# Performance work log

Hardware: AMD Instinct MI355X
Metric: run time of the kernel (lower is better)

Reference implementation:

```python
import jax, jax.numpy as jnp
import numpy as np

B, T, D, L, M = 32, 512, 512, 1024, 10


def setup_inputs() -> dict:
    key = jax.random.key(0)
    ks = jax.random.split(key, 9)
    s = 1.0 / np.sqrt(D)  # torch default uniform init bound
    u = lambda k, sh: jax.random.uniform(k, sh, jnp.float32, -s, s)
    return {
        "input_h_c": jax.random.normal(ks[0], (B, T, D), jnp.float32),
        "memory": jax.random.normal(ks[1], (B, L, D), jnp.float32),
        "input_lengths": jax.random.randint(ks[2], (B,), 1, L + 1),
        "W_ih": u(ks[3], (4 * D, 2 * D)),
        "W_hh": u(ks[4], (4 * D, D)),
        "b_ih": u(ks[5], (4 * D,)),
        "b_hh": u(ks[6], (4 * D,)),
        "W_g": u(ks[7], (3 * M, D)),
        "b_g": u(ks[8], (3 * M,)),
    }


def reference(input_h_c, memory, input_lengths, W_ih, W_hh, b_ih, b_hh, W_g, b_g):
    Bq, Tq, Dq = input_h_c.shape
    Lq = memory.shape[1]
    Mq = b_g.shape[0] // 3
    u_pos = jnp.arange(Lq, dtype=memory.dtype)  # [L]

    def step(carry, x_t):
        h, c, ctx, _ = carry
        x = jnp.concatenate([x_t, ctx], axis=-1)  # [B, 2D]
        gates = x @ W_ih.T + b_ih + h @ W_hh.T + b_hh  # [B, 4D]
        i, f, g, o = jnp.split(gates, 4, axis=-1)  # torch LSTMCell gate order i,f,g,o
        c_n = jax.nn.sigmoid(f) * c + jax.nn.sigmoid(i) * jnp.tanh(g)
        h_n = jax.nn.sigmoid(o) * jnp.tanh(c_n)
        # GMM CDF location attention
        phi = h_n @ W_g.T + b_g  # [B, 3M]
        ksi = jnp.exp(phi[:, :Mq])
        beta = jnp.exp(phi[:, Mq:2 * Mq])
        alpha = jax.nn.softmax(phi[:, 2 * Mq:], axis=-1)
        # 1/(1+exp((ksi-u)/beta)) == sigmoid((u-ksi)/beta)
        cdf = lambda ub: jnp.sum(
            alpha[..., None] * jax.nn.sigmoid((ub - ksi[..., None]) / beta[..., None]),
            axis=1)  # [B, L]
        t1 = cdf(u_pos + 0.5)
        w = t1 - cdf(u_pos - 0.5)  # [B, L]
        ctx_n = jnp.einsum('bl,bld->bd', w, memory)
        return (h_n, c_n, ctx_n, 1.0 - t1), w

    z = jnp.zeros((Bq, Dq), input_h_c.dtype)
    term0 = jnp.zeros((Bq, Lq), input_h_c.dtype)
    (h, c, ctx, term), ws = jax.lax.scan(step, (z, z, z, term0),
                                         jnp.swapaxes(input_h_c, 0, 1))
    alignment = jnp.swapaxes(ws, 0, 1)  # [B, T, L]
    termination = jnp.take_along_axis(term, (input_lengths - 1)[:, None], axis=1)  # [B,1]
    return ctx[:, None, :], alignment, termination
```

## Files before the change

kernel.cpp:

```cpp
#include <hip/hip_runtime.h>

#define Bz 32
#define Tz 512
#define Dz 512
#define Lz 1024
#define Mz 10
#define G4D 2048
#define FP 32
#define NBQ 4
#define NBLK (Bz*NBQ)
#define OFF_FQ   0
#define OFF_HX   4096
#define OFF_WQ   36864
#define OFF_M2   561152
#define OFF_XW   34115584
#define NEED_I   50892800
#define PM 128
#define PN 128
#define PK 32

typedef unsigned long long u64;
typedef unsigned u32;
typedef _Float16 f16x8 __attribute__((ext_vector_type(8)));
typedef float f32x4 __attribute__((ext_vector_type(4)));
typedef _Float16 half2_t __attribute__((ext_vector_type(2)));

#if defined(__has_builtin)
#if __has_builtin(__builtin_amdgcn_fdot2)
#define HAS_FDOT2 1
#endif
#endif

__device__ __forceinline__ float fsig(float x) { return 1.0f / (1.0f + __expf(-x)); }
__device__ __forceinline__ int ld_rlx(const int* p) {
  return __hip_atomic_load(p, __ATOMIC_RELAXED, __HIP_MEMORY_SCOPE_AGENT);
}
__device__ __forceinline__ void st_rlx(int* p, int v) {
  __hip_atomic_store(p, v, __ATOMIC_RELAXED, __HIP_MEMORY_SCOPE_AGENT);
}
__device__ __forceinline__ float ld_rlxf(const float* p) {
  return __hip_atomic_load(p, __ATOMIC_RELAXED, __HIP_MEMORY_SCOPE_AGENT);
}
__device__ __forceinline__ void st_rlxf(float* p, float v) {
  __hip_atomic_store(p, v, __ATOMIC_RELAXED, __HIP_MEMORY_SCOPE_AGENT);
}
__device__ __forceinline__ u32 pack16(float a, float b) {
  unsigned short la = __builtin_bit_cast(unsigned short, (_Float16)a);
  unsigned short lb = __builtin_bit_cast(unsigned short, (_Float16)b);
  return (u32)la | ((u32)lb << 16);
}
__device__ __forceinline__ float lo16(u32 v) {
  return (float)__builtin_bit_cast(half2_t, v)[0];
}
__device__ __forceinline__ float hi16(u32 v) {
  return (float)__builtin_bit_cast(half2_t, v)[1];
}
__device__ __forceinline__ float dot2f(u32 xu, u32 wu, float acc) {
  half2_t xh = __builtin_bit_cast(half2_t, xu);
  half2_t wh = __builtin_bit_cast(half2_t, wu);
#ifdef HAS_FDOT2
  return __builtin_amdgcn_fdot2(xh, wh, acc, false);
#else
  return acc + (float)xh[0]*(float)wh[0] + (float)xh[1]*(float)wh[1];
#endif
}
#define VWAIT() asm volatile("s_waitcnt vmcnt(0)" ::: "memory")

__global__ __launch_bounds__(256) void k_pre(
    const float* __restrict__ x, const float* __restrict__ W_ih,
    const float* __restrict__ b_ih, const float* __restrict__ b_hh,
    u32* __restrict__ xwu)
{
  __shared__ float As[PM][PK+1];
  __shared__ float Bs[PN][PK+1];
  const int m0 = blockIdx.x*PM, n0 = blockIdx.y*PN;
  const int tid = threadIdx.x;
  const int mg = tid >> 4, ng = tid & 15;
  float acc[8][8] = {};
  for (int k0 = 0; k0 < Dz; k0 += PK) {
    for (int i = tid; i < PM*(PK/4); i += 256) {
      int row = i >> 3, c4 = (i & 7) << 2;
      float4 v = *reinterpret_cast<const float4*>(&x[(size_t)(m0+row)*Dz + k0 + c4]);
      As[row][c4] = v.x; As[row][c4+1] = v.y; As[row][c4+2] = v.z; As[row][c4+3] = v.w;
    }
    for (int i = tid; i < PN*(PK/4); i += 256) {
      int row = i >> 3, c4 = (i & 7) << 2;
      float4 v = *reinterpret_cast<const float4*>(&W_ih[(size_t)(n0+row)*(2*Dz) + k0 + c4]);
      Bs[row][c4] = v.x; Bs[row][c4+1] = v.y; Bs[row][c4+2] = v.z; Bs[row][c4+3] = v.w;
    }
    __syncthreads();
    #pragma unroll 8
    for (int k = 0; k < PK; k++) {
      float a8[8], b8[8];
      #pragma unroll
      for (int r = 0; r < 8; r++) a8[r] = As[mg*8+r][k];
      #pragma unroll
      for (int s = 0; s < 8; s++) b8[s] = Bs[ng*8+s][k];
      #pragma unroll
      for (int r = 0; r < 8; r++)
        #pragma unroll
        for (int s = 0; s < 8; s++) acc[r][s] += a8[r]*b8[s];
    }
    __syncthreads();
  }
  const int nb = n0 + ng*8;
  #pragma unroll
  for (int r = 0; r < 8; r++) {
    int m = m0 + mg*8 + r;
    #pragma unroll
    for (int s2 = 0; s2 < 4; s2++) {
      int n = nb + 2*s2;
      xwu[(size_t)m*1024 + (n >> 1)] =
          pack16(acc[r][2*s2]   + b_ih[n]   + b_hh[n],
                 acc[r][2*s2+1] + b_ih[n+1] + b_hh[n+1]);
    }
  }
}

__global__ __launch_bounds__(512) void k_m2(
    const float* __restrict__ memory, const float* __restrict__ W_ih,
    u32* __restrict__ M2u)
{
  __shared__ __align__(16) u32 smem[149760/4];
  u32* Bs = smem;
  u32* As = smem + 33280;
  const int tid = threadIdx.x;
  const int n0 = blockIdx.x * 128, mc = blockIdx.y;
  for (int i = tid; i < 128*256; i += 512) {
    int jl = i >> 8, ku = i & 255;
    float2 wv = *reinterpret_cast<const float2*>(&W_ih[(size_t)(n0+jl)*(2*Dz) + 512 + 2*ku]);
    Bs[jl*260 + (ku ^ ((jl & 7) << 2))] = pack16(wv.x, wv.y);
  }
  __syncthreads();
  const int w = tid >> 6, lane = tid & 63;
  const int fr = lane & 15, kq = (lane >> 4) << 2;
  const int frsw = (fr & 7) << 2;
  for (int mt = 0; mt < 128; ++mt) {
    const int m0 = mc*2048 + mt*16;
    for (int i = tid; i < 16*256; i += 512) {
      int r = i >> 8, ku = i & 255;
      float2 mv = *reinterpret_cast<const float2*>(&memory[(size_t)(m0+r)*Dz + 2*ku]);
      As[r*260 + (ku ^ ((r & 7) << 2))] = pack16(mv.x, mv.y);
    }
    __syncthreads();
    f32x4 acc = {0.f, 0.f, 0.f, 0.f};
    #pragma unroll
    for (int ks = 0; ks < 16; ++ks) {
      int col = (kq + ks*16) ^ frsw;
      f16x8 av = *reinterpret_cast<const f16x8*>(As + fr*260 + col);
      f16x8 bv = *reinterpret_cast<const f16x8*>(Bs + (w*16 + fr)*260 + col);
      acc = __builtin_amdgcn_mfma_f32_16x16x32_f16(av, bv, acc, 0, 0, 0);
    }
    #pragma unroll
    for (int i = 0; i < 4; ++i) {
      float oth = __shfl_xor(acc[i], 1);
      if (!(lane & 1)) {
        int m = m0 + ((lane >> 4) << 2) + i;
        int j = n0 + w*16 + fr;
        M2u[(size_t)m*1024 + (j >> 1)] = pack16(acc[i], oth);
      }
    }
    __syncthreads();
  }
}

__global__ __launch_bounds__(512) void k_packh(
    const float* __restrict__ W_hh, u32* __restrict__ Wq)
{
  const int kp = blockIdx.x;
  for (int idx = threadIdx.x; idx < 2048; idx += 512) {
    int q = idx >> 9, pos = idx & 511;
    int g = pos >> 7, jj = pos & 127;
    int j = 512*g + 128*q + jj;
    float2 wv = *reinterpret_cast<const float2*>(&W_hh[(size_t)j*Dz + 2*kp]);
    Wq[(((size_t)q*256 + kp) << 9) + pos] = pack16(wv.x, wv.y);
  }
}

__global__ __launch_bounds__(512) void k_persist(
    const float* __restrict__ memory, const int* __restrict__ lens,
    const float* __restrict__ W_g,  const float* __restrict__ b_g,
    const u32* __restrict__ xwu, const u32* __restrict__ M2u,
    const u32* __restrict__ Wq,
    float* __restrict__ hx, int* __restrict__ fQ,
    float* __restrict__ ctx_out, float* __restrict__ align_out,
    float* __restrict__ term_out)
{
  const int blk = blockIdx.x, tid = threadIdx.x;
  const int b = blk >> 2, q = blk & 3;

  __shared__ float pgemv[4][512];
  __shared__ float gctxl[512];
  __shared__ float wsm[Lz];
  __shared__ float hf[Dz];
  __shared__ float cs[128];
  __shared__ u32   xp[256];
  __shared__ float2 pg2[2][256];
  __shared__ float phis[3*Mz], prm[3*Mz], lom[Mz], him[Mz];
  __shared__ int rng[2];

  if (tid < 128) cs[tid] = 0.f;
  if (tid < 256) xp[tid] = 0u;
  for (int i = tid; i < 512; i += 512) gctxl[i] = 0.f;
  __syncthreads();

  const uint4* wq4 = reinterpret_cast<const uint4*>(Wq) + (size_t)q*32768;
  const int kg = tid >> 7, tq = tid & 127;

  for (int t = 0; t < Tz; ++t) {
    {
      const uint4* wr = wq4 + tq;
      float a0 = 0.f, a1 = 0.f, a2 = 0.f, a3 = 0.f;
      const int k0 = kg << 6;
      #pragma unroll 4
      for (int kp = k0; kp < k0 + 64; ++kp) {
        uint4 wv = wr[(size_t)kp << 7];
        u32 xv = xp[kp];
        a0 = dot2f(xv, wv.x, a0);
        a1 = dot2f(xv, wv.y, a1);
        a2 = dot2f(xv, wv.z, a2);
        a3 = dot2f(xv, wv.w, a3);
      }
      *reinterpret_cast<float4*>(&pgemv[kg][tq << 2]) = make_float4(a0, a1, a2, a3);
    }
    __syncthreads();

    if (tid < 128) {
      const int dl = tid;
      const size_t xwb = ((size_t)(b*Tz + t)) << 10;
      float gv[4];
      #pragma unroll
      for (int g = 0; g < 4; ++g) {
        int pos = (g << 7) + dl;
        float s = pgemv[0][pos] + pgemv[1][pos] + pgemv[2][pos] + pgemv[3][pos]
                + gctxl[pos];
        int j = (g << 9) + (q << 7) + dl;
        u32 xv = xwu[xwb + (j >> 1)];
        s += (j & 1) ? hi16(xv) : lo16(xv);
        gv[g] = s;
      }
      float ig = fsig(gv[0]);
      float fg = fsig(gv[1]);
      float gg = tanhf(gv[2]);
      float og = fsig(gv[3]);
      float cn = fg*cs[dl] + ig*gg;
      float hn = og*tanhf(cn);
      cs[dl] = cn;
      hf[(q << 7) + dl] = hn;
      st_rlxf(&hx[(((t & 1)*Bz + b)*NBQ + q)*128 + dl], hn);
    }
    VWAIT();
    __syncthreads();
    if (tid == 0) st_rlx(&fQ[(b*NBQ + q)*FP], t+1);

    if (tid < NBQ) {
      while (ld_rlx(&fQ[(b*NBQ + tid)*FP]) < t+1) __builtin_amdgcn_s_sleep(1);
    }
    __syncthreads();
    if (tid < 384) {
      int rp = tid >> 7;
      int p = rp + (rp >= q ? 1 : 0);
      int dl2 = tid & 127;
      hf[(p << 7) + dl2] = ld_rlxf(&hx[(((t & 1)*Bz + b)*NBQ + p)*128 + dl2]);
    }
    __syncthreads();
    if (tid < 256) xp[tid] = pack16(hf[2*tid], hf[2*tid+1]);

    if (tid < 16*3*Mz) {
      int m = tid >> 4, l16 = tid & 15;
      const float4* wr = reinterpret_cast<const float4*>(W_g + m*Dz);
      const float4* hr = reinterpret_cast<const float4*>(hf);
      float s = 0.f;
      #pragma unroll
      for (int i = 0; i < 8; i++) {
        float4 wv = wr[l16 + (i<<4)];
        float4 hv = hr[l16 + (i<<4)];
        s += wv.x*hv.x + wv.y*hv.y + wv.z*hv.z + wv.w*hv.w;
      }
      s += __shfl_xor(s, 1);
      s += __shfl_xor(s, 2);
      s += __shfl_xor(s, 4);
      s += __shfl_xor(s, 8);
      if (l16 == 0) phis[m] = s + b_g[m];
    }
    __syncthreads();

    if (tid < Mz) {
      float ks = expf(phis[tid]);
      float be = expf(phis[Mz + tid]);
      prm[tid]      = ks;
      prm[Mz + tid] = expf(-phis[Mz + tid]);
      lom[tid] = ks - 0.5f - 25.f*be;
      him[tid] = ks + 0.5f + 25.f*be;
    }
    __syncthreads();
    if (tid == 0) {
      float mx = -1e30f;
      #pragma unroll
      for (int m = 0; m < Mz; m++) mx = fmaxf(mx, phis[2*Mz + m]);
      float ae[Mz], ssum = 0.f;
      #pragma unroll
      for (int m = 0; m < Mz; m++) { ae[m] = expf(phis[2*Mz + m] - mx); ssum += ae[m]; }
      float lo = 1e30f, hi = -1e30f;
      #pragma unroll
      for (int m = 0; m < Mz; m++) {
        prm[2*Mz + m] = ae[m] / ssum;
        lo = fminf(lo, lom[m]); hi = fmaxf(hi, him[m]);
      }
      int llo = lo > 0.f ? (int)floorf(lo) : 0;
      if (llo > Lz) llo = Lz;
      int lhi = hi < (float)Lz ? (int)ceilf(hi) + 1 : Lz;
      if (lhi > Lz) lhi = Lz;
      rng[0] = llo; rng[1] = lhi;
    }
    __syncthreads();
    const int llo = rng[0], lhi = rng[1];

    for (int l = llo + tid; l < lhi; l += 512) {
      float u = (float)l;
      float t1 = 0.f, t0 = 0.f;
      #pragma unroll
      for (int m = 0; m < Mz; m++) {
        float ks = prm[m], ib = prm[Mz + m], al = prm[2*Mz + m];
        t1 += al * fsig((u + 0.5f - ks) * ib);
        t0 += al * fsig((u - 0.5f - ks) * ib);
      }
      wsm[l] = t1 - t0;
    }
    __syncthreads();

    if (t < Tz-1) {
      {
        const int seg = tid >> 8, tc = tid & 255;
        const int g = tc >> 6, jj2 = tc & 63;
        const int col = (g << 8) + (q << 6) + jj2;
        const u32* m2c = M2u + (((size_t)b << 10) << 10) + col;
        float alo = 0.f, ahi = 0.f;
        for (int l = llo + seg; l < lhi; l += 2) {
          float wl = wsm[l];
          u32 v = m2c[(size_t)l << 10];
          alo = fmaf(wl, lo16(v), alo);
          ahi = fmaf(wl, hi16(v), ahi);
        }
        pg2[seg][tc] = make_float2(alo, ahi);
      }
      __syncthreads();
      if (tid < 256) {
        float2 v0 = pg2[0][tid], v1 = pg2[1][tid];
        int g = tid >> 6, jj2 = tid & 63;
        gctxl[(g << 7) + 2*jj2]     = v0.x + v1.x;
        gctxl[(g << 7) + 2*jj2 + 1] = v0.y + v1.y;
      }
      __syncthreads();
    } else if (q == 0) {
      {
        const int grp = tid >> 7, d0 = (tid & 127) << 2;
        const float* mb = memory + (size_t)b*Lz*Dz + d0;
        float4 a = make_float4(0.f, 0.f, 0.f, 0.f);
        for (int l = llo + grp; l < lhi; l += 4) {
          float wl = wsm[l];
          float4 m0 = *reinterpret_cast<const float4*>(&mb[(size_t)l*Dz]);
          a.x = fmaf(wl, m0.x, a.x); a.y = fmaf(wl, m0.y, a.y);
          a.z = fmaf(wl, m0.z, a.z); a.w = fmaf(wl, m0.w, a.w);
        }
        *reinterpret_cast<float4*>(&pgemv[grp][d0]) = a;
      }
      __syncthreads();
      ctx_out[b*Dz + tid] = pgemv[0][tid] + pgemv[1][tid] + pgemv[2][tid] + pgemv[3][tid];
      if (tid == 0) {
        float u = (float)(lens[b] - 1);
        float t1 = 0.f;
        #pragma unroll
        for (int m = 0; m < Mz; m++)
          t1 += prm[2*Mz + m] * fsig((u + 0.5f - prm[m]) * prm[Mz + m]);
        term_out[b] = 1.0f - t1;
      }
    }

    if (q == 0) {
      for (int l = llo + tid; l < lhi; l += 512)
        align_out[((size_t)b*Tz + t)*Lz + l] = wsm[l];
    }
  }
}

__global__ __launch_bounds__(256) void k_gemm(
    const float* __restrict__ x_all, const float* __restrict__ ctxs,
    const float* __restrict__ h, const float* __restrict__ W_ih,
    const float* __restrict__ W_hh, float* __restrict__ partial, int t)
{
  __shared__ float Xs[Bz][130];
  __shared__ float Wt[128][130];
  const int jt = blockIdx.x, kcb = blockIdx.y;
  const int j0 = jt*128, k0 = kcb*128;
  const int tid = threadIdx.x;
  for (int i = tid; i < Bz*128; i += 256) {
    int bb = i >> 7, kk = i & 127;
    int k = k0 + kk;
    float v;
    if (k < Dz)        v = x_all[((size_t)bb*Tz + t)*Dz + k];
    else if (k < 2*Dz) v = ctxs[bb*Dz + (k - Dz)];
    else               v = h[bb*Dz + (k - 2*Dz)];
    Xs[bb][kk] = v;
  }
  {
    const float* Wsrc; int ldw, col0;
    if (k0 < 2*Dz) { Wsrc = W_ih; ldw = 2*Dz; col0 = k0; }
    else           { Wsrc = W_hh; ldw = Dz;   col0 = k0 - 2*Dz; }
    for (int i = tid; i < 128*32; i += 256) {
      int jj = i >> 5, k4 = (i & 31) << 2;
      float4 v = *reinterpret_cast<const float4*>(&Wsrc[(size_t)(j0 + jj)*ldw + col0 + k4]);
      Wt[jj][k4] = v.x; Wt[jj][k4+1] = v.y; Wt[jj][k4+2] = v.z; Wt[jj][k4+3] = v.w;
    }
  }
  __syncthreads();
  const int jg = tid & 31, bg = tid >> 5;
  const int bl = bg << 2;
  float acc[4][4] = {};
  #pragma unroll 4
  for (int k = 0; k < 128; k += 2) {
    float2 xv[4], wv[4];
    #pragma unroll
    for (int b2 = 0; b2 < 4; b2++)
      xv[b2] = *reinterpret_cast<const float2*>(&Xs[bl + b2][k]);
    #pragma unroll
    for (int jj = 0; jj < 4; jj++)
      wv[jj] = *reinterpret_cast<const float2*>(&Wt[jg + (jj << 5)][k]);
    #pragma unroll
    for (int jj = 0; jj < 4; jj++)
      #pragma unroll
      for (int b2 = 0; b2 < 4; b2++)
        acc[jj][b2] += wv[jj].x * xv[b2].x + wv[jj].y * xv[b2].y;
  }
  #pragma unroll
  for (int jj = 0; jj < 4; jj++)
    #pragma unroll
    for (int b2 = 0; b2 < 4; b2++)
      partial[((size_t)kcb*Bz + (bl + b2))*G4D + j0 + jg + (jj << 5)] = acc[jj][b2];
}

__global__ __launch_bounds__(512) void k_fused(
    const float* __restrict__ partial, const float* __restrict__ b_ih,
    const float* __restrict__ b_hh,
    float* __restrict__ h, float* __restrict__ c,
    const float* __restrict__ W_g, const float* __restrict__ b_g,
    const float* __restrict__ memory, const int* __restrict__ lens,
    float* __restrict__ ctxs, float* __restrict__ ctx_out,
    float* __restrict__ align_out, float* __restrict__ term_out,
    int t, int final_, int nkc)
{
  const int b = blockIdx.x, tid = threadIdx.x;
  __shared__ float4 gs4[G4D/4];
  __shared__ float hsb[Dz];
  __shared__ float phis[3*Mz];
  __shared__ float prm[3*Mz];
  __shared__ float wsm[Lz];
  __shared__ int   rng[2];
  float* gs = (float*)gs4;
  {
    int j = 4*tid;
    float4 bi = *reinterpret_cast<const float4*>(&b_ih[j]);
    float4 bh = *reinterpret_cast<const float4*>(&b_hh[j]);
    float4 s = make_float4(bi.x+bh.x, bi.y+bh.y, bi.z+bh.z, bi.w+bh.w);
    const float4* pp = reinterpret_cast<const float4*>(partial) + (size_t)b*(G4D/4) + tid;
    for (int kcb = 0; kcb < nkc; kcb++) {
      float4 p = pp[(size_t)kcb*Bz*(G4D/4)];
      s.x += p.x; s.y += p.y; s.z += p.z; s.w += p.w;
    }
    gs4[tid] = s;
  }
  __syncthreads();
  {
    const int d = tid;
    float ig = 1.0f / (1.0f + expf(-gs[d]));
    float fg = 1.0f / (1.0f + expf(-gs[Dz + d]));
    float gg = tanhf(gs[2*Dz + d]);
    float og = 1.0f / (1.0f + expf(-gs[3*Dz + d]));
    float cn = fg * c[b*Dz + d] + ig * gg;
    float hn = og * tanhf(cn);
    c[b*Dz + d] = cn;
    h[b*Dz + d] = hn;
    hsb[d] = hn;
  }
  __syncthreads();
  if (tid < 16*3*Mz) {
    int m = tid >> 4, l16 = tid & 15;
    float s = 0.f;
    #pragma unroll 4
    for (int k = l16; k < Dz; k += 16) s += W_g[m*Dz + k] * hsb[k];
    s += __shfl_xor(s, 1);
    s += __shfl_xor(s, 2);
    s += __shfl_xor(s, 4);
    s += __shfl_xor(s, 8);
    if (l16 == 0) phis[m] = s + b_g[m];
  }
  __syncthreads();
  if (tid == 0) {
    float mx = -1e30f;
    #pragma unroll
    for (int m = 0; m < Mz; m++) mx = fmaxf(mx, phis[2*Mz + m]);
    float ae[Mz], ssum = 0.f;
    #pragma unroll
    for (int m = 0; m < Mz; m++) { ae[m] = expf(phis[2*Mz + m] - mx); ssum += ae[m]; }
    float lo = 1e30f, hi = -1e30f;
    #pragma unroll
    for (int m = 0; m < Mz; m++) {
      float ks = expf(phis[m]);
      float be = expf(phis[Mz + m]);
      prm[m]        = ks;
      prm[Mz + m]   = expf(-phis[Mz + m]);
      prm[2*Mz + m] = ae[m] / ssum;
      lo = fminf(lo, ks - 0.5f - 25.f*be);
      hi = fmaxf(hi, ks + 0.5f + 25.f*be);
    }
    int llo = lo > 0.f ? (int)floorf(lo) : 0;
    if (llo > Lz) llo = Lz;
    int lhi = hi < (float)Lz ? (int)ceilf(hi) + 1 : Lz;
    if (lhi > Lz) lhi = Lz;
    rng[0] = llo; rng[1] = lhi;
  }
  __syncthreads();
  const int llo = rng[0], lhi = rng[1];
  for (int l = llo + tid; l < lhi; l += 512) {
    float u = (float)l;
    float t1 = 0.f, t0 = 0.f;
    #pragma unroll
    for (int m = 0; m < Mz; m++) {
      float ks = prm[m], ib = prm[Mz + m], al = prm[2*Mz + m];
      t1 += al * fsig((u + 0.5f - ks) * ib);
      t0 += al * fsig((u - 0.5f - ks) * ib);
    }
    float w = t1 - t0;
    wsm[l] = w;
    align_out[((size_t)b*Tz + t)*Lz + l] = w;
  }
  __syncthreads();
  {
    const float* mb = memory + (size_t)b*Lz*Dz + tid;
    float acc = 0.f;
    #pragma unroll 4
    for (int l = llo; l < lhi; l++)
      acc += wsm[l] * mb[(size_t)l*Dz];
    ctxs[b*Dz + tid] = acc;
    if (final_) ctx_out[b*Dz + tid] = acc;
  }
  if (final_ && tid == 0) {
    float u = (float)(lens[b] - 1);
    float t1 = 0.f;
    #pragma unroll
    for (int m = 0; m < Mz; m++)
      t1 += prm[2*Mz + m] * fsig((u + 0.5f - prm[m]) * prm[Mz + m]);
    term_out[b] = 1.0f - t1;
  }
}

extern "C" void kernel_launch(void* const* d_in, const int* in_sizes, int n_in,
                              void* d_out, int out_size, void* d_ws, size_t ws_size,
                              hipStream_t stream)
{
  (void)in_sizes; (void)n_in; (void)out_size;
  const float* x    = (const float*)d_in[0];
  const float* mem  = (const float*)d_in[1];
  const int*   lens = (const int*)d_in[2];
  const float* W_ih = (const float*)d_in[3];
  const float* W_hh = (const float*)d_in[4];
  const float* b_ih = (const float*)d_in[5];
  const float* b_hh = (const float*)d_in[6];
  const float* W_g  = (const float*)d_in[7];
  const float* b_g  = (const float*)d_in[8];

  float* out = (float*)d_out;
  float* ctx_out   = out;
  float* align_out = out + Bz*Dz;
  float* term_out  = out + Bz*Dz + (size_t)Bz*Tz*Lz;

  const size_t needP = (size_t)NEED_I * sizeof(int);

  hipMemsetAsync(align_out, 0, (size_t)Bz*Tz*Lz*sizeof(float), stream);

  if (ws_size >= needP) {
    int*   ip  = (int*)d_ws;
    int*   fQ  = ip + OFF_FQ;
    float* hx  = (float*)(ip + OFF_HX);
    u32*   Wq  = (u32*)(ip + OFF_WQ);
    u32*   M2u = (u32*)(ip + OFF_M2);
    u32*   xwu = (u32*)(ip + OFF_XW);

    hipMemsetAsync(d_ws, 0, (size_t)OFF_HX * sizeof(int), stream);
    k_pre<<<dim3((Bz*Tz)/PM, G4D/PN), 256, 0, stream>>>(x, W_ih, b_ih, b_hh, xwu);
    k_m2<<<dim3(16, 16), 512, 0, stream>>>(mem, W_ih, M2u);
    k_packh<<<256, 512, 0, stream>>>(W_hh, Wq);
    k_persist<<<NBLK, 512, 0, stream>>>(mem, lens, W_g, b_g, xwu, M2u, Wq,
                                        hx, fQ, ctx_out, align_out, term_out);
  } else {
    float* wsf     = (float*)d_ws;
    float* h       = wsf;
    float* c       = h + Bz*Dz;
    float* ctxs    = c + Bz*Dz;
    float* partial = ctxs + Bz*Dz;
    hipMemsetAsync(d_ws, 0, (size_t)(3*Bz*Dz)*sizeof(float), stream);
    for (int t = 0; t < Tz; t++) {
      k_gemm<<<dim3(G4D/128, 12), 256, 0, stream>>>(x, ctxs, h, W_ih, W_hh, partial, t);
      k_fused<<<Bz, 512, 0, stream>>>(partial, b_ih, b_hh, h, c, W_g, b_g,
                                      mem, lens, ctxs, ctx_out, align_out, term_out,
                                      t, t == Tz-1, 12);
    }
  }
}
```

Before: 6.719 ms.

## Overlap recurrent GEMV with previous step's attention via warp-specialized halves

Splits the 512-thread block into two halves: the first 256 threads do the W_hh GEMV for step t, while the other 256 threads concurrently compute the GMM attention, the alignment weights and the memory-context gate contribution for step t-1. The halves coordinate through LDS atomic counters instead of full barriers. The final step's attention and context readout moves after the loop, and the xw loads are prefetched into registers at the start of each step. This aims to take the attention work off the serial critical path of each timestep. In exchange the GEMV runs on half the threads, and correctness now depends on the custom spin-wait synchronization.

Result: faster. 6.027 ms (-10.3%).

```diff
diff --git a/kernel.cpp b/kernel.cpp
--- a/kernel.cpp
+++ b/kernel.cpp
@@ -177,6 +177,15 @@
   }
 }
 
+#define HSYNC(id, tgt) do {                                                    \
+  __threadfence_block();                                                       \
+  if ((tid & 63) == 0) atomicAdd(&scnt[id], 1);                                \
+  while (__hip_atomic_load(&scnt[id], __ATOMIC_RELAXED,                        \
+                           __HIP_MEMORY_SCOPE_WORKGROUP) < (tgt))              \
+    __builtin_amdgcn_s_sleep(1);                                               \
+  __threadfence_block();                                                       \
+} while (0)
+
 __global__ __launch_bounds__(512) void k_persist(
     const float* __restrict__ memory, const int* __restrict__ lens,
     const float* __restrict__ W_g,  const float* __restrict__ b_g,
@@ -195,25 +204,36 @@
   __shared__ float hf[Dz];
   __shared__ float cs[128];
   __shared__ u32   xp[256];
-  __shared__ float2 pg2[2][256];
-  __shared__ float phis[3*Mz], prm[3*Mz], lom[Mz], him[Mz];
-  __shared__ int rng[2];
+  __shared__ float phis[3*Mz], prm[3*Mz];
+  __shared__ int   rng[2];
+  __shared__ int   scnt[3];
 
   if (tid < 128) cs[tid] = 0.f;
   if (tid < 256) xp[tid] = 0u;
-  for (int i = tid; i < 512; i += 512) gctxl[i] = 0.f;
+  if (tid < 3)   scnt[tid] = 0;
+  gctxl[tid] = 0.f;
   __syncthreads();
 
   const uint4* wq4 = reinterpret_cast<const uint4*>(Wq) + (size_t)q*32768;
-  const int kg = tid >> 7, tq = tid & 127;
 
   for (int t = 0; t < Tz; ++t) {
-    {
-      const uint4* wr = wq4 + tq;
+    u32 xwp0 = 0, xwp1 = 0, xwp2 = 0, xwp3 = 0;
+    if (tid < 128) {
+      const size_t xwb = ((size_t)(b*Tz + t)) << 10;
+      const int o = (q << 6) + (tid >> 1);
+      xwp0 = xwu[xwb + o];
+      xwp1 = xwu[xwb + 256 + o];
+      xwp2 = xwu[xwb + 512 + o];
+      xwp3 = xwu[xwb + 768 + o];
+    }
+
+    if (tid < 256) {
+      const int kg2 = tid >> 7, tq2 = tid & 127;
+      const uint4* wr = wq4 + tq2;
       float a0 = 0.f, a1 = 0.f, a2 = 0.f, a3 = 0.f;
-      const int k0 = kg << 6;
+      const int k0 = kg2 << 7;
       #pragma unroll 4
-      for (int kp = k0; kp < k0 + 64; ++kp) {
+      for (int kp = k0; kp < k0 + 128; ++kp) {
         uint4 wv = wr[(size_t)kp << 7];
         u32 xv = xp[kp];
         a0 = dot2f(xv, wv.x, a0);
@@ -221,22 +241,101 @@
         a2 = dot2f(xv, wv.z, a2);
         a3 = dot2f(xv, wv.w, a3);
       }
-      *reinterpret_cast<float4*>(&pgemv[kg][tq << 2]) = make_float4(a0, a1, a2, a3);
+      *reinterpret_cast<float4*>(&pgemv[kg2][tq2 << 2]) = make_float4(a0, a1, a2, a3);
+    } else if (t > 0) {
+      const int t2 = tid - 256;
+      const int tgt = 4 * t;
+      if (t2 < 8*3*Mz) {
+        int m = t2 >> 3, l8 = t2 & 7;
+        const float4* wr2 = reinterpret_cast<const float4*>(W_g + m*Dz);
+        const float4* hr = reinterpret_cast<const float4*>(hf);
+        float s = 0.f;
+        #pragma unroll
+        for (int i = 0; i < 16; i++) {
+          float4 wv = wr2[l8 + (i << 3)];
+          float4 hv = hr[l8 + (i << 3)];
+          s += wv.x*hv.x + wv.y*hv.y + wv.z*hv.z + wv.w*hv.w;
+        }
+        s += __shfl_xor(s, 1);
+        s += __shfl_xor(s, 2);
+        s += __shfl_xor(s, 4);
+        if (l8 == 0) phis[m] = s + b_g[m];
+      }
+      HSYNC(0, tgt);
+      if (t2 == 0) {
+        float mx = -1e30f;
+        #pragma unroll
+        for (int m = 0; m < Mz; m++) mx = fmaxf(mx, phis[2*Mz + m]);
+        float ae[Mz], ssum = 0.f;
+        #pragma unroll
+        for (int m = 0; m < Mz; m++) { ae[m] = expf(phis[2*Mz + m] - mx); ssum += ae[m]; }
+        float lo = 1e30f, hi = -1e30f;
+        #pragma unroll
+        for (int m = 0; m < Mz; m++) {
+          float ks = expf(phis[m]);
+          float be = expf(phis[Mz + m]);
+          prm[m]        = ks;
+          prm[Mz + m]   = expf(-phis[Mz + m]);
+          prm[2*Mz + m] = ae[m] / ssum;
+          lo = fminf(lo, ks - 0.5f - 25.f*be);
+          hi = fmaxf(hi, ks + 0.5f + 25.f*be);
+        }
+        int llo = lo > 0.f ? (int)floorf(lo) : 0;
+        if (llo > Lz) llo = Lz;
+        int lhi = hi < (float)Lz ? (int)ceilf(hi) + 1 : Lz;
+        if (lhi > Lz) lhi = Lz;
+        rng[0] = llo; rng[1] = lhi;
+      }
+      HSYNC(1, tgt);
+      const int llo = rng[0], lhi = rng[1];
+      for (int l = llo + t2; l < lhi; l += 256) {
+        float u = (float)l;
+        float t1 = 0.f, t0 = 0.f;
+        #pragma unroll
+        for (int m = 0; m < Mz; m++) {
+          float ks = prm[m], ib = prm[Mz + m], al = prm[2*Mz + m];
+          t1 += al * fsig((u + 0.5f - ks) * ib);
+          t0 += al * fsig((u - 0.5f - ks) * ib);
+        }
+        wsm[l] = t1 - t0;
+      }
+      HSYNC(2, tgt);
+      {
+        const int g = t2 >> 6, jj2 = t2 & 63;
+        const int col = (g << 8) + (q << 6) + jj2;
+        const u32* m2c = M2u + (((size_t)b << 10) << 10) + col;
+        float alo0 = 0.f, ahi0 = 0.f, alo1 = 0.f, ahi1 = 0.f;
+        int l = llo;
+        for (; l + 1 < lhi; l += 2) {
+          float w0 = wsm[l], w1 = wsm[l+1];
+          u32 v0 = m2c[(size_t)l << 10];
+          u32 v1 = m2c[(size_t)(l+1) << 10];
+          alo0 = fmaf(w0, lo16(v0), alo0); ahi0 = fmaf(w0, hi16(v0), ahi0);
+          alo1 = fmaf(w1, lo16(v1), alo1); ahi1 = fmaf(w1, hi16(v1), ahi1);
+        }
+        if (l < lhi) {
+          float w0 = wsm[l]; u32 v0 = m2c[(size_t)l << 10];
+          alo0 = fmaf(w0, lo16(v0), alo0); ahi0 = fmaf(w0, hi16(v0), ahi0);
+        }
+        gctxl[(g << 7) + 2*jj2]     = alo0 + alo1;
+        gctxl[(g << 7) + 2*jj2 + 1] = ahi0 + ahi1;
+      }
+      if (q == 0) {
+        for (int l = llo + t2; l < lhi; l += 256)
+          align_out[((size_t)b*Tz + (t-1))*Lz + l] = wsm[l];
+      }
     }
     __syncthreads();
 
     if (tid < 128) {
       const int dl = tid;
-      const size_t xwb = ((size_t)(b*Tz + t)) << 10;
+      u32 xwp[4] = {xwp0, xwp1, xwp2, xwp3};
       float gv[4];
       #pragma unroll
       for (int g = 0; g < 4; ++g) {
         int pos = (g << 7) + dl;
-        float s = pgemv[0][pos] + pgemv[1][pos] + pgemv[2][pos] + pgemv[3][pos]
-                + gctxl[pos];
-        int j = (g << 9) + (q << 7) + dl;
-        u32 xv = xwu[xwb + (j >> 1)];
-        s += (j & 1) ? hi16(xv) : lo16(xv);
+        float s = pgemv[0][pos] + pgemv[1][pos] + gctxl[pos];
+        s += (dl & 1) ? hi16(xwp[g]) : lo16(xwp[g]);
         gv[g] = s;
       }
       float ig = fsig(gv[0]);
@@ -265,122 +364,89 @@
     }
     __syncthreads();
     if (tid < 256) xp[tid] = pack16(hf[2*tid], hf[2*tid+1]);
-
-    if (tid < 16*3*Mz) {
-      int m = tid >> 4, l16 = tid & 15;
-      const float4* wr = reinterpret_cast<const float4*>(W_g + m*Dz);
-      const float4* hr = reinterpret_cast<const float4*>(hf);
-      float s = 0.f;
-      #pragma unroll
-      for (int i = 0; i < 8; i++) {
-        float4 wv = wr[l16 + (i<<4)];
-        float4 hv = hr[l16 + (i<<4)];
-        s += wv.x*hv.x + wv.y*hv.y + wv.z*hv.z + wv.w*hv.w;
-      }
-      s += __shfl_xor(s, 1);
-      s += __shfl_xor(s, 2);
-      s += __shfl_xor(s, 4);
-      s += __shfl_xor(s, 8);
-      if (l16 == 0) phis[m] = s + b_g[m];
-    }
-    __syncthreads();
-
-    if (tid < Mz) {
-      float ks = expf(phis[tid]);
-      float be = expf(phis[Mz + tid]);
-      prm[tid]      = ks;
-      prm[Mz + tid] = expf(-phis[Mz + tid]);
-      lom[tid] = ks - 0.5f - 25.f*be;
-      him[tid] = ks + 0.5f + 25.f*be;
-    }
-    __syncthreads();
-    if (tid == 0) {
-      float mx = -1e30f;
-      #pragma unroll
-      for (int m = 0; m < Mz; m++) mx = fmaxf(mx, phis[2*Mz + m]);
-      float ae[Mz], ssum = 0.f;
-      #pragma unroll
-      for (int m = 0; m < Mz; m++) { ae[m] = expf(phis[2*Mz + m] - mx); ssum += ae[m]; }
-      float lo = 1e30f, hi = -1e30f;
-      #pragma unroll
-      for (int m = 0; m < Mz; m++) {
-        prm[2*Mz + m] = ae[m] / ssum;
-        lo = fminf(lo, lom[m]); hi = fmaxf(hi, him[m]);
-      }
-      int llo = lo > 0.f ? (int)floorf(lo) : 0;
-      if (llo > Lz) llo = Lz;
-      int lhi = hi < (float)Lz ? (int)ceilf(hi) + 1 : Lz;
-      if (lhi > Lz) lhi = Lz;
-      rng[0] = llo; rng[1] = lhi;
-    }
-    __syncthreads();
-    const int llo = rng[0], lhi = rng[1];
-
-    for (int l = llo + tid; l < lhi; l += 512) {
-      float u = (float)l;
-      float t1 = 0.f, t0 = 0.f;
-      #pragma unroll
-      for (int m = 0; m < Mz; m++) {
-        float ks = prm[m], ib = prm[Mz + m], al = prm[2*Mz + m];
-        t1 += al * fsig((u + 0.5f - ks) * ib);
-        t0 += al * fsig((u - 0.5f - ks) * ib);
-      }
-      wsm[l] = t1 - t0;
-    }
-    __syncthreads();
-
-    if (t < Tz-1) {
-      {
-        const int seg = tid >> 8, tc = tid & 255;
-        const int g = tc >> 6, jj2 = tc & 63;
-        const int col = (g << 8) + (q << 6) + jj2;
-        const u32* m2c = M2u + (((size_t)b << 10) << 10) + col;
-        float alo = 0.f, ahi = 0.f;
-        for (int l = llo + seg; l < lhi; l += 2) {
-          float wl = wsm[l];
-          u32 v = m2c[(size_t)l << 10];
-          alo = fmaf(wl, lo16(v), alo);
-          ahi = fmaf(wl, hi16(v), ahi);
-        }
-        pg2[seg][tc] = make_float2(alo, ahi);
-      }
-      __syncthreads();
-      if (tid < 256) {
-        float2 v0 = pg2[0][tid], v1 = pg2[1][tid];
-        int g = tid >> 6, jj2 = tid & 63;
-        gctxl[(g << 7) + 2*jj2]     = v0.x + v1.x;
-        gctxl[(g << 7) + 2*jj2 + 1] = v0.y + v1.y;
-      }
-      __syncthreads();
-    } else if (q == 0) {
-      {
-        const int grp = tid >> 7, d0 = (tid & 127) << 2;
-        const float* mb = memory + (size_t)b*Lz*Dz + d0;
-        float4 a = make_float4(0.f, 0.f, 0.f, 0.f);
-        for (int l = llo + grp; l < lhi; l += 4) {
-          float wl = wsm[l];
-          float4 m0 = *reinterpret_cast<const float4*>(&mb[(size_t)l*Dz]);
-          a.x = fmaf(wl, m0.x, a.x); a.y = fmaf(wl, m0.y, a.y);
-          a.z = fmaf(wl, m0.z, a.z); a.w = fmaf(wl, m0.w, a.w);
-        }
-        *reinterpret_cast<float4*>(&pgemv[grp][d0]) = a;
-      }
-      __syncthreads();
-      ctx_out[b*Dz + tid] = pgemv[0][tid] + pgemv[1][tid] + pgemv[2][tid] + pgemv[3][tid];
-      if (tid == 0) {
-        float u = (float)(lens[b] - 1);
-        float t1 = 0.f;
-        #pragma unroll
-        for (int m = 0; m < Mz; m++)
-          t1 += prm[2*Mz + m] * fsig((u + 0.5f - prm[m]) * prm[Mz + m]);
-        term_out[b] = 1.0f - t1;
-      }
-    }
-
-    if (q == 0) {
-      for (int l = llo + tid; l < lhi; l += 512)
-        align_out[((size_t)b*Tz + t)*Lz + l] = wsm[l];
-    }
+    __syncthreads();
+  }
+
+  if (q != 0) return;
+  if (tid < 16*3*Mz) {
+    int m = tid >> 4, l16 = tid & 15;
+    const float4* wr = reinterpret_cast<const float4*>(W_g + m*Dz);
+    const float4* hr = reinterpret_cast<const float4*>(hf);
+    float s = 0.f;
+    #pragma unroll
+    for (int i = 0; i < 8; i++) {
+      float4 wv = wr[l16 + (i<<4)];
+      float4 hv = hr[l16 + (i<<4)];
+      s += wv.x*hv.x + wv.y*hv.y + wv.z*hv.z + wv.w*hv.w;
+    }
+    s += __shfl_xor(s, 1);
+    s += __shfl_xor(s, 2);
+    s += __shfl_xor(s, 4);
+    s += __shfl_xor(s, 8);
+    if (l16 == 0) phis[m] = s + b_g[m];
+  }
+  __syncthreads();
+  if (tid == 0) {
+    float mx = -1e30f;
+    #pragma unroll
+    for (int m = 0; m < Mz; m++) mx = fmaxf(mx, phis[2*Mz + m]);
+    float ae[Mz], ssum = 0.f;
+    #pragma unroll
+    for (int m = 0; m < Mz; m++) { ae[m] = expf(phis[2*Mz + m] - mx); ssum += ae[m]; }
+    float lo = 1e30f, hi = -1e30f;
+    #pragma unroll
+    for (int m = 0; m < Mz; m++) {
+      float ks = expf(phis[m]);
+      float be = expf(phis[Mz + m]);
+      prm[m]        = ks;
+      prm[Mz + m]   = expf(-phis[Mz + m]);
+      prm[2*Mz + m] = ae[m] / ssum;
+      lo = fminf(lo, ks - 0.5f - 25.f*be);
+      hi = fmaxf(hi, ks + 0.5f + 25.f*be);
+    }
+    int llo = lo > 0.f ? (int)floorf(lo) : 0;
+    if (llo > Lz) llo = Lz;
+    int lhi = hi < (float)Lz ? (int)ceilf(hi) + 1 : Lz;
+    if (lhi > Lz) lhi = Lz;
+    rng[0] = llo; rng[1] = lhi;
+  }
+  __syncthreads();
+  const int llo = rng[0], lhi = rng[1];
+  for (int l = llo + tid; l < lhi; l += 512) {
+    float u = (float)l;
+    float t1 = 0.f, t0 = 0.f;
+    #pragma unroll
+    for (int m = 0; m < Mz; m++) {
+      float ks = prm[m], ib = prm[Mz + m], al = prm[2*Mz + m];
+      t1 += al * fsig((u + 0.5f - ks) * ib);
+      t0 += al * fsig((u - 0.5f - ks) * ib);
+    }
+    float w = t1 - t0;
+    wsm[l] = w;
+    align_out[((size_t)b*Tz + (Tz-1))*Lz + l] = w;
+  }
+  __syncthreads();
+  {
+    const int grp = tid >> 7, d0 = (tid & 127) << 2;
+    const float* mb = memory + (size_t)b*Lz*Dz + d0;
+    float4 a = make_float4(0.f, 0.f, 0.f, 0.f);
+    for (int l = llo + grp; l < lhi; l += 4) {
+      float wl = wsm[l];
+      float4 m0 = *reinterpret_cast<const float4*>(&mb[(size_t)l*Dz]);
+      a.x = fmaf(wl, m0.x, a.x); a.y = fmaf(wl, m0.y, a.y);
+      a.z = fmaf(wl, m0.z, a.z); a.w = fmaf(wl, m0.w, a.w);
+    }
+    *reinterpret_cast<float4*>(&pgemv[grp][d0]) = a;
+  }
+  __syncthreads();
+  ctx_out[b*Dz + tid] = pgemv[0][tid] + pgemv[1][tid] + pgemv[2][tid] + pgemv[3][tid];
+  if (tid == 0) {
+    float u = (float)(lens[b] - 1);
+    float t1 = 0.f;
+    #pragma unroll
+    for (int m = 0; m < Mz; m++)
+      t1 += prm[2*Mz + m] * fsig((u + 0.5f - prm[m]) * prm[Mz + m]);
+    term_out[b] = 1.0f - t1;
   }
 }
 
```
